# Kernel tuning notes

Measured on AMD Instinct MI355X. Metric: run time of the kernel, lower is better.

The kernel has to match this reference:

```python
import jax, jax.numpy as jnp
import numpy as np
from jax import lax

CAPACITY_FACTOR = 1.0

def setup_inputs() -> dict:
    key = jax.random.key(0)
    k1, k2 = jax.random.split(key)
    x = jax.random.normal(k1, (16384, 4096), dtype=jnp.float32)
    wg = jax.random.normal(k2, (128, 4096), dtype=jnp.float32) * (1.0 / np.sqrt(4096))
    return {"x": x, "wg": wg}


def reference(x, wg):
    # logits: [T, E]
    logits = jnp.einsum('td,ed->te', x, wg)
    T, E = logits.shape
    capacity = 2 * int(CAPACITY_FACTOR * ((T + E - 1) // E))  # static python int

    # top-2 expert indices per token
    _, top2 = lax.top_k(logits, 2)           # [T, 2]
    idx1, idx2 = top2[:, 0], top2[:, 1]       # [T]

    mask1 = jax.nn.one_hot(idx1, E, dtype=jnp.int32)  # [T, E]
    mask2 = jax.nn.one_hot(idx2, E, dtype=jnp.int32)

    gates = jax.nn.softmax(logits, axis=1)    # [T, E]
    gates1_s = jnp.sum(gates * mask1, axis=1)  # [T]
    gates2_s = jnp.sum(gates * mask2, axis=1)

    # per-expert running position (cumsum over tokens)
    locations1 = jnp.cumsum(mask1, axis=0) - 1
    locations2 = jnp.cumsum(mask2, axis=0) - 1 + jnp.sum(mask1, axis=0, keepdims=True)

    # drop tokens over capacity
    mask1 = mask1 * (locations1 < capacity).astype(jnp.int32)
    mask2 = mask2 * (locations2 < capacity).astype(jnp.int32)

    locations1_s = jnp.sum(locations1 * mask1, axis=1)  # [T]
    locations2_s = jnp.sum(locations2 * mask2, axis=1)

    # load-balancing aux loss (float32 branch of original)
    me = jnp.sum(gates, axis=0)                       # [E]
    ce = jnp.sum(mask1.astype(gates.dtype), axis=0)   # [E] (post-capacity mask)
    l_aux = jnp.sum(me * ce) * (E / (T * T))

    return (l_aux, capacity, E,
            idx1.astype(jnp.int32), idx2.astype(jnp.int32),
            locations1_s.astype(jnp.int32), locations2_s.astype(jnp.int32),
            gates1_s, gates2_s)
```

## Files before the change

### kernel.cpp

```cpp
#include <hip/hip_runtime.h>

typedef _Float16 half8 __attribute__((ext_vector_type(8)));
typedef _Float16 half4 __attribute__((ext_vector_type(4)));
typedef float    f32x4 __attribute__((ext_vector_type(4)));

#define T_TOK 16384
#define D_DIM 4096
#define E_EXP 128
#define CAP   256
#define BM    32
#define NT    32

#define A_BUF_SZ  8192
#define A_PIPE_SZ 16384

__global__ __launch_bounds__(256) void prep_wt(
    const float* __restrict__ wg, _Float16* __restrict__ wt)
{
    const int t = blockIdx.x * 256 + threadIdx.x;
    const int c = t & 3;
    const int e = (t >> 2) & 127;
    const int s = t >> 9;

    const float* src = wg + (size_t)e * D_DIM + s * 32 + c * 8;
    const f32x4 v0 = *reinterpret_cast<const f32x4*>(src);
    const f32x4 v1 = *reinterpret_cast<const f32x4*>(src + 4);

    half8 h, m;
#pragma unroll
    for (int j = 0; j < 4; j++) {
        float sv = v0[j] * 64.0f;
        _Float16 hh = (_Float16)sv;
        h[j] = hh; m[j] = (_Float16)(sv - (float)hh);
        sv = v1[j] * 64.0f;
        hh = (_Float16)sv;
        h[4 + j] = hh; m[4 + j] = (_Float16)(sv - (float)hh);
    }
    _Float16* dst = wt + (size_t)s * 8192 + e * 32 + c * 8;
    *reinterpret_cast<half8*>(dst)        = h;
    *reinterpret_cast<half8*>(dst + 4096) = m;
}

__global__ __launch_bounds__(512, 4) void gemm_gate(
    const float* __restrict__ x, const _Float16* __restrict__ wt,
    float* __restrict__ out, float* __restrict__ me, int* __restrict__ cnt1)
{
    __shared__ char smem[2 * A_PIPE_SZ];
    __shared__ float lg[BM][E_EXP + 1];

    const int tid  = threadIdx.x;
    const int row0 = blockIdx.x * BM;
    const int lane = tid & 63;
    const int w    = tid >> 6;
    const int kp   = w >> 2;
    const int wl   = w & 3;
    const int lr   = lane & 15;
    const int lq   = lane >> 4;

    const int sp   = tid >> 8;
    const int srow = (tid >> 3) & 31;
    const int sg   = tid & 7;
    const float* xA = x + (size_t)(row0 + srow) * D_DIM + sp * 2048 + sg * 4;
    const int awr_h = sp * A_PIPE_SZ + srow * 256 +
                      (((sg >> 1)    ) ^ (srow & 7)) * 16 + (sg & 1) * 8;
    const int awr_m = sp * A_PIPE_SZ + srow * 256 +
                      (((sg >> 1) | 4) ^ (srow & 7)) * 16 + (sg & 1) * 8;

    const int ah_ch = ((lq    ) ^ (lr & 7)) * 16;
    const int am_ch = ((lq | 4) ^ (lr & 7)) * 16;
    const char* const ard = smem + kp * A_PIPE_SZ;

    const _Float16* const wtB =
        wt + (size_t)(kp * 64) * 8192 + (wl * 32 + lr) * 32 + lq * 8;

    f32x4 acc[2][2];
#pragma unroll
    for (int i = 0; i < 2; i++)
#pragma unroll
        for (int j = 0; j < 2; j++) acc[i][j] = (f32x4)0.0f;

#define CONV_WRITE(av0, av1, buf)                                             \
    {                                                                         \
        half4 h0, m0, h1, m1;                                                 \
        _Pragma("unroll") for (int j = 0; j < 4; j++) {                       \
            _Float16 hh = (_Float16)av0[j];                                   \
            h0[j] = hh; m0[j] = (_Float16)(av0[j] - (float)hh);               \
            hh = (_Float16)av1[j];                                            \
            h1[j] = hh; m1[j] = (_Float16)(av1[j] - (float)hh);               \
        }                                                                     \
        char* const wb = smem + (buf) * A_BUF_SZ;                             \
        *reinterpret_cast<half4*>(wb + awr_h)       = h0;                     \
        *reinterpret_cast<half4*>(wb + awr_m)       = m0;                     \
        *reinterpret_cast<half4*>(wb + awr_h + 128) = h1;                     \
        *reinterpret_cast<half4*>(wb + awr_m + 128) = m1;                     \
    }

#define BAR()                                                                 \
    asm volatile("s_waitcnt lgkmcnt(0)" ::: "memory");                        \
    __builtin_amdgcn_sched_barrier(0);                                        \
    __builtin_amdgcn_s_barrier();                                             \
    __builtin_amdgcn_sched_barrier(0);

#define SUBSTEP(cur, ks, Bh, Bm)                                              \
    {                                                                         \
        half8 Ah[2], Am[2];                                                   \
        _Pragma("unroll") for (int rf = 0; rf < 2; rf++) {                    \
            const char* ab = ard + (cur) * A_BUF_SZ +                         \
                             (rf * 16 + lr) * 256 + (ks) * 128;               \
            Ah[rf] = *reinterpret_cast<const half8*>(ab + ah_ch);             \
            Am[rf] = *reinterpret_cast<const half8*>(ab + am_ch);             \
        }                                                                     \
        _Pragma("unroll") for (int rf = 0; rf < 2; rf++)                      \
            _Pragma("unroll") for (int cf = 0; cf < 2; cf++) {                \
                acc[rf][cf] = __builtin_amdgcn_mfma_f32_16x16x32_f16(         \
                    Am[rf], Bh[cf], acc[rf][cf], 0, 0, 0);                    \
                acc[rf][cf] = __builtin_amdgcn_mfma_f32_16x16x32_f16(         \
                    Ah[rf], Bm[cf], acc[rf][cf], 0, 0, 0);                    \
                acc[rf][cf] = __builtin_amdgcn_mfma_f32_16x16x32_f16(         \
                    Ah[rf], Bh[cf], acc[rf][cf], 0, 0, 0);                    \
            }                                                                 \
    }

#define STEP(cur, A0C, A1C, A0N, A1N, t)                                      \
    {                                                                         \
        const int kn = (((t) + 2) & (NT - 1)) * 64;                           \
        A0N = *reinterpret_cast<const f32x4*>(xA + kn);                       \
        A1N = *reinterpret_cast<const f32x4*>(xA + kn + 32);                  \
        const _Float16* bp0 = wtB + (size_t)(2 * (t)) * 8192;                 \
        half8 Bh0[2], Bm0[2], Bh1[2], Bm1[2];                                 \
        _Pragma("unroll") for (int cf = 0; cf < 2; cf++) {                    \
            Bh0[cf] = *reinterpret_cast<const half8*>(bp0 + cf * 512);        \
            Bm0[cf] = *reinterpret_cast<const half8*>(bp0 + 4096 + cf * 512); \
            Bh1[cf] = *reinterpret_cast<const half8*>(bp0 + 8192 + cf * 512); \
            Bm1[cf] = *reinterpret_cast<const half8*>(bp0 + 12288 + cf * 512);\
        }                                                                     \
        SUBSTEP(cur, 0, Bh0, Bm0);                                            \
        SUBSTEP(cur, 1, Bh1, Bm1);                                            \
        CONV_WRITE(A0C, A1C, (cur) ^ 1);                                      \
        BAR();                                                                \
    }

    f32x4 avA0, avA1, avB0, avB1;

    {
        const f32x4 a00 = *reinterpret_cast<const f32x4*>(xA);
        const f32x4 a01 = *reinterpret_cast<const f32x4*>(xA + 32);
        avA0 = *reinterpret_cast<const f32x4*>(xA + 64);
        avA1 = *reinterpret_cast<const f32x4*>(xA + 96);
        CONV_WRITE(a00, a01, 0);
        BAR();
    }

    for (int t = 0; t < NT; t += 2) {
        STEP(0, avA0, avA1, avB0, avB1, t);
        STEP(1, avB0, avB1, avA0, avA1, t + 1);
    }

#undef STEP
#undef SUBSTEP
#undef BAR
#undef CONV_WRITE

    if (kp == 1) {
#pragma unroll
        for (int rf = 0; rf < 2; rf++)
#pragma unroll
            for (int cf = 0; cf < 2; cf++)
#pragma unroll
                for (int r = 0; r < 4; r++)
                    lg[rf * 16 + lq * 4 + r][wl * 32 + cf * 16 + lr] =
                        acc[rf][cf][r] * 0.015625f;
    }
    __syncthreads();
    if (kp == 0) {
#pragma unroll
        for (int rf = 0; rf < 2; rf++)
#pragma unroll
            for (int cf = 0; cf < 2; cf++)
#pragma unroll
                for (int r = 0; r < 4; r++)
                    lg[rf * 16 + lq * 4 + r][wl * 32 + cf * 16 + lr] +=
                        acc[rf][cf][r] * 0.015625f;
    }
    __syncthreads();

    if (tid < BM) {
        const int r = tid;
        const int t = row0 + r;
        float m1 = -1e30f, m2 = -1e30f;
        int   i1 = 0, i2 = 0;
        for (int e = 0; e < E_EXP; e++) {
            const float v = lg[r][e];
            if (v > m1)      { m2 = m1; i2 = i1; m1 = v; i1 = e; }
            else if (v > m2) { m2 = v; i2 = e; }
        }
        float s = 0.0f;
        for (int e = 0; e < E_EXP; e++) s += __expf(lg[r][e] - m1);
        const float inv = 1.0f / s;

        out[3 + 0 * T_TOK + t] = (float)i1;
        out[3 + 1 * T_TOK + t] = (float)i2;
        out[3 + 4 * T_TOK + t] = inv;
        out[3 + 5 * T_TOK + t] = __expf(m2 - m1) * inv;
        atomicAdd(&cnt1[i1], 1);

        for (int e = 0; e < E_EXP; e++)
            lg[r][e] = __expf(lg[r][e] - m1) * inv;
    }
    __syncthreads();

    if (tid < E_EXP) {
        float s = 0.0f;
        for (int r = 0; r < BM; r++) s += lg[r][tid];
        atomicAdd(&me[tid], s);
    }
}

__global__ __launch_bounds__(1024) void rank_kernel(
    float* __restrict__ out, const int* __restrict__ cnt1)
{
    const int  e      = blockIdx.x & 127;
    const bool second = blockIdx.x >= 128;
    const int  tid    = threadIdx.x;
    const int  lane   = tid & 63;
    const int  w      = tid >> 6;

    __shared__ int wtot[16];

    const float* idxA = out + 3 + (second ? T_TOK : 0);
    float* loc = out + 3 + (second ? 3 * T_TOK : 2 * T_TOK);

    const unsigned long long below = (1ull << lane) - 1ull;
    int base = second ? cnt1[e] : 0;

    for (int t0 = 0; t0 < T_TOK; t0 += 1024) {
        const int t = t0 + tid;
        const int f = ((int)idxA[t] == e);
        const unsigned long long m = __ballot(f);
        const int pre = __popcll(m & below);
        const int tot = __popcll(m);
        if (lane == 0) wtot[w] = tot;
        __syncthreads();
        int off = 0, all = 0;
#pragma unroll
        for (int i = 0; i < 16; i++) {
            const int v = wtot[i];
            if (i < w) off += v;
            all += v;
        }
        if (f) {
            const int rank = base + off + pre;
            loc[t] = (rank < CAP) ? (float)rank : 0.0f;
        }
        base += all;
        __syncthreads();
    }
}

__global__ __launch_bounds__(128) void finalize_kernel(
    const float* __restrict__ me, const int* __restrict__ cnt1,
    float* __restrict__ out)
{
    __shared__ float red[2];
    const int tid = threadIdx.x;
    const int c = cnt1[tid];
    float p = me[tid] * (float)((c < CAP) ? c : CAP);
#pragma unroll
    for (int o = 32; o > 0; o >>= 1) p += __shfl_down(p, o);
    if ((tid & 63) == 0) red[tid >> 6] = p;
    __syncthreads();
    if (tid == 0) {
        const float tot = red[0] + red[1];
        out[0] = tot * ((float)E_EXP / ((float)T_TOK * (float)T_TOK));
        out[1] = (float)CAP;
        out[2] = (float)E_EXP;
    }
}

extern "C" void kernel_launch(void* const* d_in, const int* in_sizes, int n_in,
                              void* d_out, int out_size, void* d_ws, size_t ws_size,
                              hipStream_t stream)
{
    const float* x  = (const float*)d_in[0];
    const float* wg = (const float*)d_in[1];
    float* out = (float*)d_out;

    float* me   = (float*)d_ws;
    int*   cnt1 = (int*)((char*)d_ws + 512);
    _Float16* wt = (_Float16*)((char*)d_ws + 1024);

    hipMemsetAsync(d_ws, 0, 1024, stream);
    prep_wt<<<256, 256, 0, stream>>>(wg, wt);
    gemm_gate<<<T_TOK / BM, 512, 0, stream>>>(x, wt, out, me, cnt1);
    rank_kernel<<<2 * E_EXP, 1024, 0, stream>>>(out, cnt1);
    finalize_kernel<<<1, 128, 0, stream>>>(me, cnt1, out);
}
```

Before: 118.4 us.

## Deepen K-step per barrier and software-pipeline B-fragment loads in gate GEMM

Each pipeline step in the gate GEMM now covers 128 K-elements with four MFMA substeps instead of 64, which halves the number of block barriers and global A loads per row. B-fragment loads are double-buffered in registers (P/Q) so the next substep's weights are fetched while the current MFMAs run. s_setprio raises wave priority around the MFMA bursts. The logits scratch now aliases the larger A staging buffer, so total LDS stays about the same. In exchange, register pressure rises from the extra A and B vectors, which could limit occupancy at 4 blocks of 512 threads.

Result: slower. 124.0 us (+4.8%).

```diff
diff --git a/kernel.cpp b/kernel.cpp
--- a/kernel.cpp
+++ b/kernel.cpp
@@ -9,10 +9,10 @@
 #define E_EXP 128
 #define CAP   256
 #define BM    32
-#define NT    32
-
-#define A_BUF_SZ  8192
-#define A_PIPE_SZ 16384
+#define NT    16
+
+#define A_BUF_SZ  16384
+#define A_PIPE_SZ 32768
 
 __global__ __launch_bounds__(256) void prep_wt(
     const float* __restrict__ wg, _Float16* __restrict__ wt)
@@ -45,8 +45,7 @@
     const float* __restrict__ x, const _Float16* __restrict__ wt,
     float* __restrict__ out, float* __restrict__ me, int* __restrict__ cnt1)
 {
-    __shared__ char smem[2 * A_PIPE_SZ];
-    __shared__ float lg[BM][E_EXP + 1];
+    __shared__ char smem[4 * A_BUF_SZ];
 
     const int tid  = threadIdx.x;
     const int row0 = blockIdx.x * BM;
@@ -61,9 +60,9 @@
     const int srow = (tid >> 3) & 31;
     const int sg   = tid & 7;
     const float* xA = x + (size_t)(row0 + srow) * D_DIM + sp * 2048 + sg * 4;
-    const int awr_h = sp * A_PIPE_SZ + srow * 256 +
+    const int awr_h = sp * A_PIPE_SZ + srow * 512 +
                       (((sg >> 1)    ) ^ (srow & 7)) * 16 + (sg & 1) * 8;
-    const int awr_m = sp * A_PIPE_SZ + srow * 256 +
+    const int awr_m = sp * A_PIPE_SZ + srow * 512 +
                       (((sg >> 1) | 4) ^ (srow & 7)) * 16 + (sg & 1) * 8;
 
     const int ah_ch = ((lq    ) ^ (lr & 7)) * 16;
@@ -79,20 +78,27 @@
 #pragma unroll
         for (int j = 0; j < 2; j++) acc[i][j] = (f32x4)0.0f;
 
-#define CONV_WRITE(av0, av1, buf)                                             \
+#define LOAD_BSS(Bh, Bm, s)                                                   \
     {                                                                         \
-        half4 h0, m0, h1, m1;                                                 \
-        _Pragma("unroll") for (int j = 0; j < 4; j++) {                       \
-            _Float16 hh = (_Float16)av0[j];                                   \
-            h0[j] = hh; m0[j] = (_Float16)(av0[j] - (float)hh);               \
-            hh = (_Float16)av1[j];                                            \
-            h1[j] = hh; m1[j] = (_Float16)(av1[j] - (float)hh);               \
+        const _Float16* bp = wtB + (size_t)((s) & 63) * 8192;                 \
+        Bh[0] = *reinterpret_cast<const half8*>(bp);                          \
+        Bh[1] = *reinterpret_cast<const half8*>(bp + 512);                    \
+        Bm[0] = *reinterpret_cast<const half8*>(bp + 4096);                   \
+        Bm[1] = *reinterpret_cast<const half8*>(bp + 4096 + 512);             \
+    }
+
+#define CONV_WRITE(av, buf)                                                   \
+    {                                                                         \
+        _Pragma("unroll") for (int ks = 0; ks < 4; ks++) {                    \
+            half4 h, m;                                                       \
+            _Pragma("unroll") for (int j = 0; j < 4; j++) {                   \
+                const _Float16 hh = (_Float16)av[ks][j];                      \
+                h[j] = hh; m[j] = (_Float16)(av[ks][j] - (float)hh);          \
+            }                                                                 \
+            char* const wb = smem + (buf) * A_BUF_SZ + ks * 128;              \
+            *reinterpret_cast<half4*>(wb + awr_h) = h;                        \
+            *reinterpret_cast<half4*>(wb + awr_m) = m;                        \
         }                                                                     \
-        char* const wb = smem + (buf) * A_BUF_SZ;                             \
-        *reinterpret_cast<half4*>(wb + awr_h)       = h0;                     \
-        *reinterpret_cast<half4*>(wb + awr_m)       = m0;                     \
-        *reinterpret_cast<half4*>(wb + awr_h + 128) = h1;                     \
-        *reinterpret_cast<half4*>(wb + awr_m + 128) = m1;                     \
     }
 
 #define BAR()                                                                 \
@@ -106,10 +112,11 @@
         half8 Ah[2], Am[2];                                                   \
         _Pragma("unroll") for (int rf = 0; rf < 2; rf++) {                    \
             const char* ab = ard + (cur) * A_BUF_SZ +                         \
-                             (rf * 16 + lr) * 256 + (ks) * 128;               \
+                             (rf * 16 + lr) * 512 + (ks) * 128;               \
             Ah[rf] = *reinterpret_cast<const half8*>(ab + ah_ch);             \
             Am[rf] = *reinterpret_cast<const half8*>(ab + am_ch);             \
         }                                                                     \
+        __builtin_amdgcn_s_setprio(1);                                        \
         _Pragma("unroll") for (int rf = 0; rf < 2; rf++)                      \
             _Pragma("unroll") for (int cf = 0; cf < 2; cf++) {                \
                 acc[rf][cf] = __builtin_amdgcn_mfma_f32_16x16x32_f16(         \
@@ -119,48 +126,51 @@
                 acc[rf][cf] = __builtin_amdgcn_mfma_f32_16x16x32_f16(         \
                     Ah[rf], Bh[cf], acc[rf][cf], 0, 0, 0);                    \
             }                                                                 \
-    }
-
-#define STEP(cur, A0C, A1C, A0N, A1N, t)                                      \
+        __builtin_amdgcn_s_setprio(0);                                        \
+    }
+
+#define STEP(cur, t)                                                          \
     {                                                                         \
-        const int kn = (((t) + 2) & (NT - 1)) * 64;                           \
-        A0N = *reinterpret_cast<const f32x4*>(xA + kn);                       \
-        A1N = *reinterpret_cast<const f32x4*>(xA + kn + 32);                  \
-        const _Float16* bp0 = wtB + (size_t)(2 * (t)) * 8192;                 \
-        half8 Bh0[2], Bm0[2], Bh1[2], Bm1[2];                                 \
-        _Pragma("unroll") for (int cf = 0; cf < 2; cf++) {                    \
-            Bh0[cf] = *reinterpret_cast<const half8*>(bp0 + cf * 512);        \
-            Bm0[cf] = *reinterpret_cast<const half8*>(bp0 + 4096 + cf * 512); \
-            Bh1[cf] = *reinterpret_cast<const half8*>(bp0 + 8192 + cf * 512); \
-            Bm1[cf] = *reinterpret_cast<const half8*>(bp0 + 12288 + cf * 512);\
-        }                                                                     \
-        SUBSTEP(cur, 0, Bh0, Bm0);                                            \
-        SUBSTEP(cur, 1, Bh1, Bm1);                                            \
-        CONV_WRITE(A0C, A1C, (cur) ^ 1);                                      \
+        const int kn = (((t) + 1) & (NT - 1)) * 128;                          \
+        f32x4 avN[4];                                                         \
+        avN[0] = *reinterpret_cast<const f32x4*>(xA + kn);                    \
+        avN[1] = *reinterpret_cast<const f32x4*>(xA + kn + 32);               \
+        avN[2] = *reinterpret_cast<const f32x4*>(xA + kn + 64);               \
+        avN[3] = *reinterpret_cast<const f32x4*>(xA + kn + 96);               \
+        const int s0 = 4 * (t);                                               \
+        LOAD_BSS(QBh, QBm, s0 + 1);  SUBSTEP(cur, 0, PBh, PBm);               \
+        LOAD_BSS(PBh, PBm, s0 + 2);  SUBSTEP(cur, 1, QBh, QBm);               \
+        LOAD_BSS(QBh, QBm, s0 + 3);  SUBSTEP(cur, 2, PBh, PBm);               \
+        LOAD_BSS(PBh, PBm, s0 + 4);  SUBSTEP(cur, 3, QBh, QBm);               \
+        CONV_WRITE(avN, (cur) ^ 1);                                           \
         BAR();                                                                \
     }
 
-    f32x4 avA0, avA1, avB0, avB1;
+    half8 PBh[2], PBm[2], QBh[2], QBm[2];
 
     {
-        const f32x4 a00 = *reinterpret_cast<const f32x4*>(xA);
-        const f32x4 a01 = *reinterpret_cast<const f32x4*>(xA + 32);
-        avA0 = *reinterpret_cast<const f32x4*>(xA + 64);
-        avA1 = *reinterpret_cast<const f32x4*>(xA + 96);
-        CONV_WRITE(a00, a01, 0);
+        f32x4 av0[4];
+        av0[0] = *reinterpret_cast<const f32x4*>(xA);
+        av0[1] = *reinterpret_cast<const f32x4*>(xA + 32);
+        av0[2] = *reinterpret_cast<const f32x4*>(xA + 64);
+        av0[3] = *reinterpret_cast<const f32x4*>(xA + 96);
+        LOAD_BSS(PBh, PBm, 0);
+        CONV_WRITE(av0, 0);
         BAR();
     }
 
     for (int t = 0; t < NT; t += 2) {
-        STEP(0, avA0, avA1, avB0, avB1, t);
-        STEP(1, avB0, avB1, avA0, avA1, t + 1);
+        STEP(0, t);
+        STEP(1, t + 1);
     }
 
 #undef STEP
 #undef SUBSTEP
 #undef BAR
 #undef CONV_WRITE
-
+#undef LOAD_BSS
+
+    float* lg = reinterpret_cast<float*>(smem);
     if (kp == 1) {
 #pragma unroll
         for (int rf = 0; rf < 2; rf++)
@@ -168,7 +178,7 @@
             for (int cf = 0; cf < 2; cf++)
 #pragma unroll
                 for (int r = 0; r < 4; r++)
-                    lg[rf * 16 + lq * 4 + r][wl * 32 + cf * 16 + lr] =
+                    lg[(rf * 16 + lq * 4 + r) * 129 + wl * 32 + cf * 16 + lr] =
                         acc[rf][cf][r] * 0.015625f;
     }
     __syncthreads();
@@ -179,7 +189,7 @@
             for (int cf = 0; cf < 2; cf++)
 #pragma unroll
                 for (int r = 0; r < 4; r++)
-                    lg[rf * 16 + lq * 4 + r][wl * 32 + cf * 16 + lr] +=
+                    lg[(rf * 16 + lq * 4 + r) * 129 + wl * 32 + cf * 16 + lr] +=
                         acc[rf][cf][r] * 0.015625f;
     }
     __syncthreads();
@@ -190,12 +200,12 @@
         float m1 = -1e30f, m2 = -1e30f;
         int   i1 = 0, i2 = 0;
         for (int e = 0; e < E_EXP; e++) {
-            const float v = lg[r][e];
+            const float v = lg[r * 129 + e];
             if (v > m1)      { m2 = m1; i2 = i1; m1 = v; i1 = e; }
             else if (v > m2) { m2 = v; i2 = e; }
         }
         float s = 0.0f;
-        for (int e = 0; e < E_EXP; e++) s += __expf(lg[r][e] - m1);
+        for (int e = 0; e < E_EXP; e++) s += __expf(lg[r * 129 + e] - m1);
         const float inv = 1.0f / s;
 
         out[3 + 0 * T_TOK + t] = (float)i1;
@@ -205,13 +215,13 @@
         atomicAdd(&cnt1[i1], 1);
 
         for (int e = 0; e < E_EXP; e++)
-            lg[r][e] = __expf(lg[r][e] - m1) * inv;
+            lg[r * 129 + e] = __expf(lg[r * 129 + e] - m1) * inv;
     }
     __syncthreads();
 
     if (tid < E_EXP) {
         float s = 0.0f;
-        for (int r = 0; r < BM; r++) s += lg[r][tid];
+        for (int r = 0; r < BM; r++) s += lg[r * 129 + tid];
         atomicAdd(&me[tid], s);
     }
 }
```

## Double GEMM row tile to 64 with 1024-thread blocks and reuse smem for logits

Applied to the files above, without the earlier changes.

Doubles the rows per block to 64 and the threads per block to 1024. Each wave now computes a 64x16 output slice (4 row fragments × 1 expert fragment) instead of 32x32, so B fragments are reused across more rows and the total weight-matrix reads across the grid are halved. The A prefetch is reduced from two steps ahead to one, with contiguous 8-float loads, and the logit buffer now aliases the pipeline shared memory instead of taking separate LDS. The trade-offs are fewer blocks (256 on a 256-CU part), a larger per-block LDS footprint, more A LDS reads per wave, and less latency hiding on the x loads.

Result: no change. 118.3 us (-0.0%).

```diff
diff --git a/kernel.cpp b/kernel.cpp
--- a/kernel.cpp
+++ b/kernel.cpp
@@ -8,11 +8,11 @@
 #define D_DIM 4096
 #define E_EXP 128
 #define CAP   256
-#define BM    32
+#define BM    64
 #define NT    32
 
-#define A_BUF_SZ  8192
-#define A_PIPE_SZ 16384
+#define A_BUF_SZ  16384
+#define A_PIPE_SZ 32768
 
 __global__ __launch_bounds__(256) void prep_wt(
     const float* __restrict__ wg, _Float16* __restrict__ wt)
@@ -41,58 +41,53 @@
     *reinterpret_cast<half8*>(dst + 4096) = m;
 }
 
-__global__ __launch_bounds__(512, 4) void gemm_gate(
+__global__ __launch_bounds__(1024, 4) void gemm_gate(
     const float* __restrict__ x, const _Float16* __restrict__ wt,
     float* __restrict__ out, float* __restrict__ me, int* __restrict__ cnt1)
 {
     __shared__ char smem[2 * A_PIPE_SZ];
-    __shared__ float lg[BM][E_EXP + 1];
 
     const int tid  = threadIdx.x;
     const int row0 = blockIdx.x * BM;
     const int lane = tid & 63;
     const int w    = tid >> 6;
-    const int kp   = w >> 2;
-    const int wl   = w & 3;
+    const int kp   = w >> 3;
+    const int wl   = w & 7;
     const int lr   = lane & 15;
     const int lq   = lane >> 4;
 
-    const int sp   = tid >> 8;
-    const int srow = (tid >> 3) & 31;
+    const int sp   = tid >> 9;
+    const int srow = (tid >> 3) & 63;
     const int sg   = tid & 7;
-    const float* xA = x + (size_t)(row0 + srow) * D_DIM + sp * 2048 + sg * 4;
-    const int awr_h = sp * A_PIPE_SZ + srow * 256 +
-                      (((sg >> 1)    ) ^ (srow & 7)) * 16 + (sg & 1) * 8;
-    const int awr_m = sp * A_PIPE_SZ + srow * 256 +
-                      (((sg >> 1) | 4) ^ (srow & 7)) * 16 + (sg & 1) * 8;
+    const float* xA = x + (size_t)(row0 + srow) * D_DIM + sp * 2048 + sg * 8;
+    const int awr_h = sp * A_PIPE_SZ + srow * 256 + (sg >> 2) * 128 +
+                      (((sg & 3)    ) ^ (srow & 7)) * 16;
+    const int awr_m = sp * A_PIPE_SZ + srow * 256 + (sg >> 2) * 128 +
+                      (((sg & 3) | 4) ^ (srow & 7)) * 16;
 
     const int ah_ch = ((lq    ) ^ (lr & 7)) * 16;
     const int am_ch = ((lq | 4) ^ (lr & 7)) * 16;
     const char* const ard = smem + kp * A_PIPE_SZ;
 
     const _Float16* const wtB =
-        wt + (size_t)(kp * 64) * 8192 + (wl * 32 + lr) * 32 + lq * 8;
-
-    f32x4 acc[2][2];
-#pragma unroll
-    for (int i = 0; i < 2; i++)
-#pragma unroll
-        for (int j = 0; j < 2; j++) acc[i][j] = (f32x4)0.0f;
-
-#define CONV_WRITE(av0, av1, buf)                                             \
+        wt + (size_t)(kp * 64) * 8192 + (wl * 16 + lr) * 32 + lq * 8;
+
+    f32x4 acc[4];
+#pragma unroll
+    for (int i = 0; i < 4; i++) acc[i] = (f32x4)0.0f;
+
+#define CONV_WRITE(a0, a1, buf)                                               \
     {                                                                         \
-        half4 h0, m0, h1, m1;                                                 \
+        half8 h, m;                                                           \
         _Pragma("unroll") for (int j = 0; j < 4; j++) {                       \
-            _Float16 hh = (_Float16)av0[j];                                   \
-            h0[j] = hh; m0[j] = (_Float16)(av0[j] - (float)hh);               \
-            hh = (_Float16)av1[j];                                            \
-            h1[j] = hh; m1[j] = (_Float16)(av1[j] - (float)hh);               \
+            _Float16 hh = (_Float16)a0[j];                                    \
+            h[j] = hh; m[j] = (_Float16)(a0[j] - (float)hh);                  \
+            hh = (_Float16)a1[j];                                             \
+            h[4 + j] = hh; m[4 + j] = (_Float16)(a1[j] - (float)hh);          \
         }                                                                     \
         char* const wb = smem + (buf) * A_BUF_SZ;                             \
-        *reinterpret_cast<half4*>(wb + awr_h)       = h0;                     \
-        *reinterpret_cast<half4*>(wb + awr_m)       = m0;                     \
-        *reinterpret_cast<half4*>(wb + awr_h + 128) = h1;                     \
-        *reinterpret_cast<half4*>(wb + awr_m + 128) = m1;                     \
+        *reinterpret_cast<half8*>(wb + awr_h) = h;                            \
+        *reinterpret_cast<half8*>(wb + awr_m) = m;                            \
     }
 
 #define BAR()                                                                 \
@@ -101,59 +96,49 @@
     __builtin_amdgcn_s_barrier();                                             \
     __builtin_amdgcn_sched_barrier(0);
 
-#define SUBSTEP(cur, ks, Bh, Bm)                                              \
+#define SUBSTEP(cur, ks, t)                                                   \
     {                                                                         \
-        half8 Ah[2], Am[2];                                                   \
-        _Pragma("unroll") for (int rf = 0; rf < 2; rf++) {                    \
+        const _Float16* bp = wtB + (size_t)((2 * (t) + (ks)) & 63) * 8192;    \
+        const half8 Bh = *reinterpret_cast<const half8*>(bp);                 \
+        const half8 Bm = *reinterpret_cast<const half8*>(bp + 4096);          \
+        half8 Ah[4], Am[4];                                                   \
+        _Pragma("unroll") for (int rf = 0; rf < 4; rf++) {                    \
             const char* ab = ard + (cur) * A_BUF_SZ +                         \
                              (rf * 16 + lr) * 256 + (ks) * 128;               \
             Ah[rf] = *reinterpret_cast<const half8*>(ab + ah_ch);             \
             Am[rf] = *reinterpret_cast<const half8*>(ab + am_ch);             \
         }                                                                     \
-        _Pragma("unroll") for (int rf = 0; rf < 2; rf++)                      \
-            _Pragma("unroll") for (int cf = 0; cf < 2; cf++) {                \
-                acc[rf][cf] = __builtin_amdgcn_mfma_f32_16x16x32_f16(         \
-                    Am[rf], Bh[cf], acc[rf][cf], 0, 0, 0);                    \
-                acc[rf][cf] = __builtin_amdgcn_mfma_f32_16x16x32_f16(         \
-                    Ah[rf], Bm[cf], acc[rf][cf], 0, 0, 0);                    \
-                acc[rf][cf] = __builtin_amdgcn_mfma_f32_16x16x32_f16(         \
-                    Ah[rf], Bh[cf], acc[rf][cf], 0, 0, 0);                    \
-            }                                                                 \
-    }
-
-#define STEP(cur, A0C, A1C, A0N, A1N, t)                                      \
+        _Pragma("unroll") for (int rf = 0; rf < 4; rf++) {                    \
+            acc[rf] = __builtin_amdgcn_mfma_f32_16x16x32_f16(                 \
+                Am[rf], Bh, acc[rf], 0, 0, 0);                                \
+            acc[rf] = __builtin_amdgcn_mfma_f32_16x16x32_f16(                 \
+                Ah[rf], Bm, acc[rf], 0, 0, 0);                                \
+            acc[rf] = __builtin_amdgcn_mfma_f32_16x16x32_f16(                 \
+                Ah[rf], Bh, acc[rf], 0, 0, 0);                                \
+        }                                                                     \
+    }
+
+#define STEP(cur, t)                                                          \
     {                                                                         \
-        const int kn = (((t) + 2) & (NT - 1)) * 64;                           \
-        A0N = *reinterpret_cast<const f32x4*>(xA + kn);                       \
-        A1N = *reinterpret_cast<const f32x4*>(xA + kn + 32);                  \
-        const _Float16* bp0 = wtB + (size_t)(2 * (t)) * 8192;                 \
-        half8 Bh0[2], Bm0[2], Bh1[2], Bm1[2];                                 \
-        _Pragma("unroll") for (int cf = 0; cf < 2; cf++) {                    \
-            Bh0[cf] = *reinterpret_cast<const half8*>(bp0 + cf * 512);        \
-            Bm0[cf] = *reinterpret_cast<const half8*>(bp0 + 4096 + cf * 512); \
-            Bh1[cf] = *reinterpret_cast<const half8*>(bp0 + 8192 + cf * 512); \
-            Bm1[cf] = *reinterpret_cast<const half8*>(bp0 + 12288 + cf * 512);\
-        }                                                                     \
-        SUBSTEP(cur, 0, Bh0, Bm0);                                            \
-        SUBSTEP(cur, 1, Bh1, Bm1);                                            \
-        CONV_WRITE(A0C, A1C, (cur) ^ 1);                                      \
+        const int kn = (((t) + 1) & (NT - 1)) * 64;                           \
+        const f32x4 a0 = *reinterpret_cast<const f32x4*>(xA + kn);            \
+        const f32x4 a1 = *reinterpret_cast<const f32x4*>(xA + kn + 4);        \
+        SUBSTEP(cur, 0, t);                                                   \
+        SUBSTEP(cur, 1, t);                                                   \
+        CONV_WRITE(a0, a1, (cur) ^ 1);                                        \
         BAR();                                                                \
     }
 
-    f32x4 avA0, avA1, avB0, avB1;
-
     {
-        const f32x4 a00 = *reinterpret_cast<const f32x4*>(xA);
-        const f32x4 a01 = *reinterpret_cast<const f32x4*>(xA + 32);
-        avA0 = *reinterpret_cast<const f32x4*>(xA + 64);
-        avA1 = *reinterpret_cast<const f32x4*>(xA + 96);
-        CONV_WRITE(a00, a01, 0);
+        const f32x4 a0 = *reinterpret_cast<const f32x4*>(xA);
+        const f32x4 a1 = *reinterpret_cast<const f32x4*>(xA + 4);
+        CONV_WRITE(a0, a1, 0);
         BAR();
     }
 
     for (int t = 0; t < NT; t += 2) {
-        STEP(0, avA0, avA1, avB0, avB1, t);
-        STEP(1, avB0, avB1, avA0, avA1, t + 1);
+        STEP(0, t);
+        STEP(1, t + 1);
     }
 
 #undef STEP
@@ -161,26 +146,23 @@
 #undef BAR
 #undef CONV_WRITE
 
+    float* lg = reinterpret_cast<float*>(smem);
     if (kp == 1) {
 #pragma unroll
-        for (int rf = 0; rf < 2; rf++)
-#pragma unroll
-            for (int cf = 0; cf < 2; cf++)
-#pragma unroll
-                for (int r = 0; r < 4; r++)
-                    lg[rf * 16 + lq * 4 + r][wl * 32 + cf * 16 + lr] =
-                        acc[rf][cf][r] * 0.015625f;
+        for (int rf = 0; rf < 4; rf++)
+#pragma unroll
+            for (int r = 0; r < 4; r++)
+                lg[(rf * 16 + lq * 4 + r) * 129 + wl * 16 + lr] =
+                    acc[rf][r] * 0.015625f;
     }
     __syncthreads();
     if (kp == 0) {
 #pragma unroll
-        for (int rf = 0; rf < 2; rf++)
-#pragma unroll
-            for (int cf = 0; cf < 2; cf++)
-#pragma unroll
-                for (int r = 0; r < 4; r++)
-                    lg[rf * 16 + lq * 4 + r][wl * 32 + cf * 16 + lr] +=
-                        acc[rf][cf][r] * 0.015625f;
+        for (int rf = 0; rf < 4; rf++)
+#pragma unroll
+            for (int r = 0; r < 4; r++)
+                lg[(rf * 16 + lq * 4 + r) * 129 + wl * 16 + lr] +=
+                    acc[rf][r] * 0.015625f;
     }
     __syncthreads();
 
@@ -190,12 +172,12 @@
         float m1 = -1e30f, m2 = -1e30f;
         int   i1 = 0, i2 = 0;
         for (int e = 0; e < E_EXP; e++) {
-            const float v = lg[r][e];
+            const float v = lg[r * 129 + e];
             if (v > m1)      { m2 = m1; i2 = i1; m1 = v; i1 = e; }
             else if (v > m2) { m2 = v; i2 = e; }
         }
         float s = 0.0f;
-        for (int e = 0; e < E_EXP; e++) s += __expf(lg[r][e] - m1);
+        for (int e = 0; e < E_EXP; e++) s += __expf(lg[r * 129 + e] - m1);
         const float inv = 1.0f / s;
 
         out[3 + 0 * T_TOK + t] = (float)i1;
@@ -205,13 +187,13 @@
         atomicAdd(&cnt1[i1], 1);
 
         for (int e = 0; e < E_EXP; e++)
-            lg[r][e] = __expf(lg[r][e] - m1) * inv;
+            lg[r * 129 + e] = __expf(lg[r * 129 + e] - m1) * inv;
     }
     __syncthreads();
 
     if (tid < E_EXP) {
         float s = 0.0f;
-        for (int r = 0; r < BM; r++) s += lg[r][tid];
+        for (int r = 0; r < BM; r++) s += lg[r * 129 + tid];
         atomicAdd(&me[tid], s);
     }
 }
@@ -291,7 +273,7 @@
 
     hipMemsetAsync(d_ws, 0, 1024, stream);
     prep_wt<<<256, 256, 0, stream>>>(wg, wt);
-    gemm_gate<<<T_TOK / BM, 512, 0, stream>>>(x, wt, out, me, cnt1);
+    gemm_gate<<<T_TOK / BM, 1024, 0, stream>>>(x, wt, out, me, cnt1);
     rank_kernel<<<2 * E_EXP, 1024, 0, stream>>>(out, cnt1);
     finalize_kernel<<<1, 128, 0, stream>>>(me, cnt1, out);
 }
```
